# Performance work log

Measured on AMD Instinct MI355X. Metric: run time of the kernel, lower is better.

## Reference

```python
import jax, jax.numpy as jnp
import numpy as np

FP4_E2M1_VALUES = jnp.array([0.0, 0.5, 1.0, 1.5, 2.0, 3.0, 4.0, 6.0,
                             -0.0, -0.5, -1.0, -1.5, -2.0, -3.0, -4.0, -6.0],
                            dtype=jnp.float32)

OUT_F, IN_F, BS = 4096, 4096, 16


def setup_inputs() -> dict:
    key = jax.random.key(0)
    k1, k2, k3, k4 = jax.random.split(key, 4)
    x = jax.random.normal(k1, (4, 2048, IN_F), dtype=jnp.float32)
    weight_indices = jax.random.randint(k2, (OUT_F, IN_F // BS, BS), 0, 16, dtype=jnp.int32)
    weight_scales = jax.random.uniform(k3, (OUT_F, IN_F // BS), dtype=jnp.float32)
    bias = jax.random.normal(k4, (OUT_F,), dtype=jnp.float32)
    return {"x": x, "weight_indices": weight_indices,
            "weight_scales": weight_scales, "bias": bias}


def reference(x, weight_indices, weight_scales, bias):
    # Dequantize: gather FP4 values per index, scale per block of 16.
    idx = jnp.clip(weight_indices, 0, 15)              # [O, NB, BS]
    vals = FP4_E2M1_VALUES[idx]                        # [O, NB, BS]
    weight = (vals * weight_scales[:, :, None]).reshape(OUT_F, IN_F)
    # F.linear: y = x @ W^T + b
    return jnp.einsum('bsi,oi->bso', x, weight) + bias
```

## Files before the change

### kernel.cpp

```cpp
#include <hip/hip_runtime.h>
#include <hip/hip_bf16.h>

static constexpr int M_TOT = 8192;
static constexpr int N_TOT = 4096;
static constexpr int K_TOT = 4096;

static constexpr int BM = 256, BN = 256;
static constexpr int GTHREADS = 512;
static constexpr int LDS_BYTES = 131072;

typedef __bf16 bf16x8 __attribute__((ext_vector_type(8)));
typedef float f32x4 __attribute__((ext_vector_type(4)));
typedef unsigned short u16x8 __attribute__((ext_vector_type(8)));

__device__ __forceinline__ unsigned short f2bf(float f) {
  return __builtin_bit_cast(unsigned short, (__bf16)f);
}

__device__ __forceinline__ float fp4_decode(int idx) {
  unsigned u = (unsigned)idx & 15u;
  unsigned sgn = (u >> 3) << 31;
  unsigned mag = u & 7u;
  unsigned e = mag >> 1, m = mag & 1u;
  unsigned bits = (e == 0u) ? (m ? 0x3F000000u : 0u)
                            : (((126u + e) << 23) | (m << 22));
  return __uint_as_float(bits | sgn);
}

__device__ __forceinline__ void glds16(const void* g, void* l) {
  __builtin_amdgcn_global_load_lds(
      (__attribute__((address_space(1))) void*)g,
      (__attribute__((address_space(3))) void*)l, 16, 0, 0);
}

__global__ __launch_bounds__(256) void dequant_w_kernel(
    const int* __restrict__ idx, const float* __restrict__ scales,
    unsigned short* __restrict__ W) {
  const int t = blockIdx.x * 256 + threadIdx.x;
  const int4 v = reinterpret_cast<const int4*>(idx)[t];
  const float s = scales[t >> 2];
  ushort4 o;
  o.x = f2bf(fp4_decode(v.x) * s);
  o.y = f2bf(fp4_decode(v.y) * s);
  o.z = f2bf(fp4_decode(v.z) * s);
  o.w = f2bf(fp4_decode(v.w) * s);
  reinterpret_cast<ushort4*>(W)[t] = o;
}

__global__ __launch_bounds__(256) void convert_x_kernel(
    const float* __restrict__ x, unsigned short* __restrict__ A) {
  const int t = blockIdx.x * 256 + threadIdx.x;
  const float4* xp = reinterpret_cast<const float4*>(x);
  const float4 a = xp[2 * t], b = xp[2 * t + 1];
  u16x8 o;
  o[0] = f2bf(a.x); o[1] = f2bf(a.y); o[2] = f2bf(a.z); o[3] = f2bf(a.w);
  o[4] = f2bf(b.x); o[5] = f2bf(b.y); o[6] = f2bf(b.z); o[7] = f2bf(b.w);
  reinterpret_cast<u16x8*>(A)[t] = o;
}

__global__ __launch_bounds__(GTHREADS, 1) void gemm256(
    const unsigned short* __restrict__ A, const unsigned short* __restrict__ B,
    const float* __restrict__ bias, float* __restrict__ out) {
  extern __shared__ char smem[];

  const int t = threadIdx.x;
  const int lane = t & 63, wid = t >> 6;
  const int wr = wid >> 2;
  const int wc = wid & 3;
  const int l15 = lane & 15;

  const int bid = blockIdx.x;
  const int bmi = (bid & 7) * 4 + ((bid >> 3) & 3);
  const int bni = bid >> 5;
  const int bm0 = bmi * BM, bn0 = bni * BN;

  const int row_s = t >> 2;
  const int kcd = (t & 3) ^ ((t >> 3) & 3);
  const unsigned short* pA = A + (size_t)(bm0 + row_s) * K_TOT + kcd * 8;
  const unsigned short* pB = B + (size_t)(bn0 + row_s) * K_TOT + kcd * 8;
  char* stA = smem + t * 16;
  char* stB = smem + 32768 + t * 16;

  const int swz = ((lane >> 4) ^ ((l15 >> 1) & 3)) * 16;
  const int base_a = (wr * 128 + l15) * 64 + swz;
  const int base_b = 32768 + (wc * 64 + l15) * 64 + swz;

  f32x4 acc[8][4];
#pragma unroll
  for (int i = 0; i < 8; ++i)
#pragma unroll
    for (int j = 0; j < 4; ++j) acc[i][j] = f32x4{0.f, 0.f, 0.f, 0.f};

  bf16x8 afQ[4], bfQ[4];

#define STG_A(T, s, doff) do {                                           \
    const unsigned short* p_ = pA + (T) * 64 + (s) * 32;                 \
    glds16(p_, stA + (doff) + (s) * 16384);                              \
    glds16(p_ + (size_t)128 * K_TOT, stA + (doff) + (s) * 16384 + 8192); \
  } while (0)
#define STG_B(T, s, doff) do {                                           \
    const unsigned short* p_ = pB + (T) * 64 + (s) * 32;                 \
    glds16(p_, stB + (doff) + (s) * 16384);                              \
    glds16(p_ + (size_t)128 * K_TOT, stB + (doff) + (s) * 16384 + 8192); \
  } while (0)

#define RD_A4(doff, s, mh) do {                                          \
    const char* p_ = smem + (doff) + (s) * 16384 + base_a + (mh) * 4096; \
    afQ[0] = *(const bf16x8*)(p_);                                       \
    afQ[1] = *(const bf16x8*)(p_ + 1024);                                \
    afQ[2] = *(const bf16x8*)(p_ + 2048);                                \
    afQ[3] = *(const bf16x8*)(p_ + 3072);                                \
  } while (0)
#define RD_B4(doff, s) do {                                              \
    const char* p_ = smem + (doff) + (s) * 16384 + base_b;               \
    bfQ[0] = *(const bf16x8*)(p_);                                       \
    bfQ[1] = *(const bf16x8*)(p_ + 1024);                                \
    bfQ[2] = *(const bf16x8*)(p_ + 2048);                                \
    bfQ[3] = *(const bf16x8*)(p_ + 3072);                                \
  } while (0)

#define MF16(mb) do {                                                    \
    __builtin_amdgcn_s_setprio(1);                                       \
    _Pragma("unroll")                                                    \
    for (int m_ = 0; m_ < 4; ++m_)                                       \
      _Pragma("unroll")                                                  \
      for (int n_ = 0; n_ < 4; ++n_)                                     \
        acc[(mb) + m_][n_] = __builtin_amdgcn_mfma_f32_16x16x32_bf16(    \
            afQ[m_], bfQ[n_], acc[(mb) + m_][n_], 0, 0, 0);              \
    __builtin_amdgcn_s_setprio(0);                                       \
  } while (0)

#define VM(n) asm volatile("s_waitcnt vmcnt(" #n ")" ::: "memory")
#define BAR __builtin_amdgcn_s_barrier()

  STG_B(0, 0, 0);
  STG_A(0, 0, 0);
  STG_B(0, 1, 0);
  STG_A(0, 1, 0);
  STG_B(1, 0, 65536);
  STG_A(1, 0, 65536);
  STG_B(1, 1, 65536);
  VM(10);
  BAR;

#pragma unroll 1
  for (int i = 0; i < 31; ++i) {
    const int T = 2 * i, U = 2 * i + 1;
    RD_A4(0, 0, 0); RD_B4(0, 0); STG_A(U, 1, 65536);
    BAR; MF16(0); VM(12); BAR;
    RD_A4(0, 0, 1); STG_B(T + 2, 0, 0);
    BAR; MF16(4); VM(10); BAR;
    RD_A4(0, 1, 0); RD_B4(0, 1); STG_A(T + 2, 0, 0);
    BAR; MF16(0); VM(12); BAR;
    RD_A4(0, 1, 1); STG_B(T + 2, 1, 0);
    BAR; MF16(4); VM(10); BAR;
    RD_A4(65536, 0, 0); RD_B4(65536, 0); STG_A(T + 2, 1, 0);
    BAR; MF16(0); VM(12); BAR;
    RD_A4(65536, 0, 1); STG_B(U + 2, 0, 65536);
    BAR; MF16(4); VM(10); BAR;
    RD_A4(65536, 1, 0); RD_B4(65536, 1); STG_A(U + 2, 0, 65536);
    BAR; MF16(0); VM(12); BAR;
    RD_A4(65536, 1, 1); STG_B(U + 2, 1, 65536);
    BAR; MF16(4); VM(10); BAR;
  }

  RD_A4(0, 0, 0); RD_B4(0, 0); STG_A(63, 1, 65536);
  BAR; MF16(0); VM(12); BAR;
  RD_A4(0, 0, 1);
  BAR; MF16(4); VM(8); BAR;
  RD_A4(0, 1, 0); RD_B4(0, 1);
  BAR; MF16(0); VM(8); BAR;
  RD_A4(0, 1, 1);
  BAR; MF16(4); VM(4); BAR;
  RD_A4(65536, 0, 0); RD_B4(65536, 0);
  BAR; MF16(0); VM(4); BAR;
  RD_A4(65536, 0, 1);
  BAR; MF16(4); VM(0); BAR;
  RD_A4(65536, 1, 0); RD_B4(65536, 1);
  BAR; MF16(0); BAR;
  RD_A4(65536, 1, 1);
  MF16(4);

  const int orow0 = bm0 + wr * 128 + (lane >> 4) * 4;
  const int ocol0 = bn0 + wc * 64 + l15;
  float bj[4];
#pragma unroll
  for (int n = 0; n < 4; ++n) bj[n] = bias[ocol0 + n * 16];
#pragma unroll
  for (int mi = 0; mi < 8; ++mi)
#pragma unroll
    for (int n = 0; n < 4; ++n)
#pragma unroll
      for (int q = 0; q < 4; ++q)
        out[(size_t)(orow0 + mi * 16 + q) * N_TOT + ocol0 + n * 16] =
            acc[mi][n][q] + bj[n];
}

extern "C" void kernel_launch(void* const* d_in, const int* in_sizes, int n_in,
                              void* d_out, int out_size, void* d_ws, size_t ws_size,
                              hipStream_t stream) {
  const float* x = (const float*)d_in[0];
  const int* widx = (const int*)d_in[1];
  const float* wsc = (const float*)d_in[2];
  const float* bias = (const float*)d_in[3];
  float* out = (float*)d_out;

  unsigned short* Abf = (unsigned short*)d_ws;
  unsigned short* Wbf = (unsigned short*)((char*)d_ws + (size_t)M_TOT * K_TOT * 2);

  convert_x_kernel<<<dim3((M_TOT * (size_t)K_TOT / 8) / 256), dim3(256), 0, stream>>>(x, Abf);
  dequant_w_kernel<<<dim3((N_TOT * (size_t)K_TOT / 4) / 256), dim3(256), 0, stream>>>(widx, wsc, Wbf);

  (void)hipFuncSetAttribute((const void*)gemm256,
                            hipFuncAttributeMaxDynamicSharedMemorySize, LDS_BYTES);
  gemm256<<<dim3((M_TOT / BM) * (N_TOT / BN)), dim3(GTHREADS), LDS_BYTES, stream>>>(
      Abf, Wbf, bias, out);
}
```

Measured before the change: 282.2 us.

## Merge prepass kernels and wait on global loads once per half-tile

The x-conversion and weight-dequant kernels become a single launch that branches on block index, which removes one kernel launch and the gap between launches. The GEMM main loop stops issuing a vmcnt wait in every sub-step. It now waits only at the end of each half K-tile (VM(6)), so more global-to-LDS loads can be in flight while MFMAs run. The cost is coarser synchronization. The scheme relies on the new wait counts still guaranteeing that each buffer is fully loaded before it is read, which is easy to get wrong.

```diff
diff --git a/kernel.cpp b/kernel.cpp
--- a/kernel.cpp
+++ b/kernel.cpp
@@ -8,6 +8,7 @@
 static constexpr int BM = 256, BN = 256;
 static constexpr int GTHREADS = 512;
 static constexpr int LDS_BYTES = 131072;
+static constexpr int D1 = 65536;
 
 typedef __bf16 bf16x8 __attribute__((ext_vector_type(8)));
 typedef float f32x4 __attribute__((ext_vector_type(4)));
@@ -33,29 +34,30 @@
       (__attribute__((address_space(3))) void*)l, 16, 0, 0);
 }
 
-__global__ __launch_bounds__(256) void dequant_w_kernel(
+__global__ __launch_bounds__(256) void prepass_kernel(
+    const float* __restrict__ x, unsigned short* __restrict__ A,
     const int* __restrict__ idx, const float* __restrict__ scales,
     unsigned short* __restrict__ W) {
-  const int t = blockIdx.x * 256 + threadIdx.x;
-  const int4 v = reinterpret_cast<const int4*>(idx)[t];
-  const float s = scales[t >> 2];
-  ushort4 o;
-  o.x = f2bf(fp4_decode(v.x) * s);
-  o.y = f2bf(fp4_decode(v.y) * s);
-  o.z = f2bf(fp4_decode(v.z) * s);
-  o.w = f2bf(fp4_decode(v.w) * s);
-  reinterpret_cast<ushort4*>(W)[t] = o;
-}
-
-__global__ __launch_bounds__(256) void convert_x_kernel(
-    const float* __restrict__ x, unsigned short* __restrict__ A) {
-  const int t = blockIdx.x * 256 + threadIdx.x;
-  const float4* xp = reinterpret_cast<const float4*>(x);
-  const float4 a = xp[2 * t], b = xp[2 * t + 1];
-  u16x8 o;
-  o[0] = f2bf(a.x); o[1] = f2bf(a.y); o[2] = f2bf(a.z); o[3] = f2bf(a.w);
-  o[4] = f2bf(b.x); o[5] = f2bf(b.y); o[6] = f2bf(b.z); o[7] = f2bf(b.w);
-  reinterpret_cast<u16x8*>(A)[t] = o;
+  const int b = blockIdx.x;
+  if (b < 16384) {
+    const int t = b * 256 + threadIdx.x;
+    const float4* xp = reinterpret_cast<const float4*>(x);
+    const float4 a = xp[2 * t], c = xp[2 * t + 1];
+    u16x8 o;
+    o[0] = f2bf(a.x); o[1] = f2bf(a.y); o[2] = f2bf(a.z); o[3] = f2bf(a.w);
+    o[4] = f2bf(c.x); o[5] = f2bf(c.y); o[6] = f2bf(c.z); o[7] = f2bf(c.w);
+    reinterpret_cast<u16x8*>(A)[t] = o;
+  } else {
+    const int t = (b - 16384) * 256 + threadIdx.x;
+    const int4 v = reinterpret_cast<const int4*>(idx)[t];
+    const float s = scales[t >> 2];
+    ushort4 o;
+    o.x = f2bf(fp4_decode(v.x) * s);
+    o.y = f2bf(fp4_decode(v.y) * s);
+    o.z = f2bf(fp4_decode(v.z) * s);
+    o.w = f2bf(fp4_decode(v.w) * s);
+    reinterpret_cast<ushort4*>(W)[t] = o;
+  }
 }
 
 __global__ __launch_bounds__(GTHREADS, 1) void gemm256(
@@ -137,48 +139,48 @@
   STG_A(0, 0, 0);
   STG_B(0, 1, 0);
   STG_A(0, 1, 0);
-  STG_B(1, 0, 65536);
-  STG_A(1, 0, 65536);
-  STG_B(1, 1, 65536);
-  VM(10);
+  STG_B(1, 0, D1);
+  STG_A(1, 0, D1);
+  STG_B(1, 1, D1);
+  VM(6);
   BAR;
 
 #pragma unroll 1
   for (int i = 0; i < 31; ++i) {
     const int T = 2 * i, U = 2 * i + 1;
-    RD_A4(0, 0, 0); RD_B4(0, 0); STG_A(U, 1, 65536);
-    BAR; MF16(0); VM(12); BAR;
+    RD_A4(0, 0, 0); RD_B4(0, 0); STG_A(U, 1, D1);
+    BAR; MF16(0); BAR;
     RD_A4(0, 0, 1); STG_B(T + 2, 0, 0);
-    BAR; MF16(4); VM(10); BAR;
+    BAR; MF16(4); BAR;
     RD_A4(0, 1, 0); RD_B4(0, 1); STG_A(T + 2, 0, 0);
-    BAR; MF16(0); VM(12); BAR;
+    BAR; MF16(0); BAR;
     RD_A4(0, 1, 1); STG_B(T + 2, 1, 0);
-    BAR; MF16(4); VM(10); BAR;
-    RD_A4(65536, 0, 0); RD_B4(65536, 0); STG_A(T + 2, 1, 0);
-    BAR; MF16(0); VM(12); BAR;
-    RD_A4(65536, 0, 1); STG_B(U + 2, 0, 65536);
-    BAR; MF16(4); VM(10); BAR;
-    RD_A4(65536, 1, 0); RD_B4(65536, 1); STG_A(U + 2, 0, 65536);
-    BAR; MF16(0); VM(12); BAR;
-    RD_A4(65536, 1, 1); STG_B(U + 2, 1, 65536);
-    BAR; MF16(4); VM(10); BAR;
+    BAR; MF16(4); VM(6); BAR;
+    RD_A4(D1, 0, 0); RD_B4(D1, 0); STG_A(T + 2, 1, 0);
+    BAR; MF16(0); BAR;
+    RD_A4(D1, 0, 1); STG_B(U + 2, 0, D1);
+    BAR; MF16(4); BAR;
+    RD_A4(D1, 1, 0); RD_B4(D1, 1); STG_A(U + 2, 0, D1);
+    BAR; MF16(0); BAR;
+    RD_A4(D1, 1, 1); STG_B(U + 2, 1, D1);
+    BAR; MF16(4); VM(6); BAR;
   }
 
-  RD_A4(0, 0, 0); RD_B4(0, 0); STG_A(63, 1, 65536);
-  BAR; MF16(0); VM(12); BAR;
+  RD_A4(0, 0, 0); RD_B4(0, 0); STG_A(63, 1, D1);
+  BAR; MF16(0); BAR;
   RD_A4(0, 0, 1);
-  BAR; MF16(4); VM(8); BAR;
+  BAR; MF16(4); BAR;
   RD_A4(0, 1, 0); RD_B4(0, 1);
-  BAR; MF16(0); VM(8); BAR;
+  BAR; MF16(0); BAR;
   RD_A4(0, 1, 1);
-  BAR; MF16(4); VM(4); BAR;
-  RD_A4(65536, 0, 0); RD_B4(65536, 0);
-  BAR; MF16(0); VM(4); BAR;
-  RD_A4(65536, 0, 1);
   BAR; MF16(4); VM(0); BAR;
-  RD_A4(65536, 1, 0); RD_B4(65536, 1);
-  BAR; MF16(0); BAR;
-  RD_A4(65536, 1, 1);
+  RD_A4(D1, 0, 0); RD_B4(D1, 0);
+  BAR; MF16(0); BAR;
+  RD_A4(D1, 0, 1);
+  BAR; MF16(4); BAR;
+  RD_A4(D1, 1, 0); RD_B4(D1, 1);
+  BAR; MF16(0); BAR;
+  RD_A4(D1, 1, 1);
   MF16(4);
 
   const int orow0 = bm0 + wr * 128 + (lane >> 4) * 4;
@@ -208,8 +210,7 @@
   unsigned short* Abf = (unsigned short*)d_ws;
   unsigned short* Wbf = (unsigned short*)((char*)d_ws + (size_t)M_TOT * K_TOT * 2);
 
-  convert_x_kernel<<<dim3((M_TOT * (size_t)K_TOT / 8) / 256), dim3(256), 0, stream>>>(x, Abf);
-  dequant_w_kernel<<<dim3((N_TOT * (size_t)K_TOT / 4) / 256), dim3(256), 0, stream>>>(widx, wsc, Wbf);
+  prepass_kernel<<<dim3(32768), dim3(256), 0, stream>>>(x, Abf, widx, wsc, Wbf);
 
   (void)hipFuncSetAttribute((const void*)gemm256,
                             hipFuncAttributeMaxDynamicSharedMemorySize, LDS_BYTES);
```

Result: no change. 282.5 us (+0.1%).
